# Performance work log

Measured on AMD Instinct MI355X. Metric: run time of the kernel, lower is better.

## Reference

```python
import jax, jax.numpy as jnp
import numpy as np

HIDDEN = 2048
HEADS = 16
HEAD_DIM = HIDDEN // HEADS  # 128
B, S = 2, 2048


def setup_inputs() -> dict:
    key = jax.random.key(0)
    ks = jax.random.split(key, 9)
    s_in = 1.0 / np.sqrt(HIDDEN)
    return {
        "X": jax.random.normal(ks[0], (B, S, HIDDEN), dtype=jnp.float32),
        "attention_mask": jnp.ones((B, S, S), dtype=jnp.int32),
        "Wq": jax.random.uniform(ks[1], (HIDDEN, HIDDEN), jnp.float32, -s_in, s_in),
        "bq": jax.random.uniform(ks[2], (HIDDEN,), jnp.float32, -s_in, s_in),
        "Wk": jax.random.uniform(ks[3], (HIDDEN, HEAD_DIM), jnp.float32, -s_in, s_in),
        "bk": jax.random.uniform(ks[4], (HEAD_DIM,), jnp.float32, -s_in, s_in),
        "Wv": jax.random.uniform(ks[5], (HIDDEN, HEAD_DIM), jnp.float32, -s_in, s_in),
        "bv": jax.random.uniform(ks[6], (HEAD_DIM,), jnp.float32, -s_in, s_in),
        "Wo": jax.random.uniform(ks[7], (HIDDEN, HIDDEN), jnp.float32, -s_in, s_in),
        "bo": jax.random.uniform(ks[8], (HIDDEN,), jnp.float32, -s_in, s_in),
    }


def reference(X, attention_mask, Wq, bq, Wk, bk, Wv, bv, Wo, bo):
    b, s, _ = X.shape
    # Projections
    Q = X @ Wq + bq                      # (B, S, H*D)
    K = X @ Wk + bk                      # (B, S, D)  shared across heads (MQA)
    V = X @ Wv + bv                      # (B, S, D)
    Q = Q.reshape(b, s, HEADS, HEAD_DIM).transpose(0, 2, 1, 3)  # (B, H, S, D)
    scale = 1.0 / jnp.sqrt(jnp.float32(HEAD_DIM))
    # QK^T with shared K head
    scores = jnp.einsum('bhqd,bkd->bhqk', Q, K) * scale          # (B, H, S, S)
    scores = jnp.where(attention_mask[:, None, :, :] == 0, -jnp.inf, scores)
    attn = jax.nn.softmax(scores, axis=-1)
    # dropout_rate = 0.0 (eval) -> identity
    out = jnp.einsum('bhqk,bkd->bhqd', attn, V)                  # (B, H, S, D)
    out = out.transpose(0, 2, 1, 3).reshape(b, s, HIDDEN)        # (B, S, hidden)
    return out @ Wo + bo
```

## Files before the change

kernel.cpp:

```cpp
#include <hip/hip_runtime.h>
#include <cstdint>
#include <cstddef>

#define HIDDEN 2048
#define HEADS 16
#define HD 128
#define BSZ 2
#define SEQ 2048
#define MTOT (BSZ * SEQ)
#define NQKV (HIDDEN + 2 * HD)
#define SL2E 0.12751743f

typedef unsigned short ushort_t;
typedef __attribute__((ext_vector_type(8))) __bf16 bf16x8;
typedef __attribute__((ext_vector_type(4))) float f32x4;

typedef __attribute__((address_space(3))) unsigned int as3_u32;
typedef __attribute__((address_space(1))) const unsigned int as1_u32;

__device__ __forceinline__ ushort_t f2bf(float x) {
  union { float f; unsigned u; } v; v.f = x;
  unsigned r = v.u + 0x7fffu + ((v.u >> 16) & 1u);
  return (ushort_t)(r >> 16);
}
__device__ __forceinline__ ushort_t f2bf_trunc(float x) {
  union { float f; unsigned u; } v; v.f = x;
  return (ushort_t)(v.u >> 16);
}

__device__ __forceinline__ void gld16(const void* g, void* lds) {
  __builtin_amdgcn_global_load_lds((as1_u32*)g, (as3_u32*)lds, 16, 0, 0);
}

__global__ __launch_bounds__(256) void cvt_bf16_kernel(
    const float* __restrict__ in, ushort_t* __restrict__ out, int n4) {
  int i = blockIdx.x * 256 + threadIdx.x;
  if (i >= n4) return;
  float4 v = ((const float4*)in)[i];
  ushort4 o;
  o.x = f2bf(v.x); o.y = f2bf(v.y); o.z = f2bf(v.z); o.w = f2bf(v.w);
  ((ushort4*)out)[i] = o;
}

__global__ __launch_bounds__(256) void cvtT_qkv_kernel(
    const float* __restrict__ Wq, const float* __restrict__ Wk,
    const float* __restrict__ Wv, ushort_t* __restrict__ WT) {
  __shared__ float tile[32][36];
  const int t = threadIdx.x;
  const int nb = blockIdx.x * 32, kb = blockIdx.y * 32;
  const float* W; int N, nc; float scale;
  if (nb < HIDDEN)            { W = Wq; N = HIDDEN; nc = nb;               scale = SL2E; }
  else if (nb < HIDDEN + HD)  { W = Wk; N = HD;     nc = nb - HIDDEN;      scale = 1.f; }
  else                        { W = Wv; N = HD;     nc = nb - HIDDEN - HD; scale = 1.f; }
  {
    int row = t >> 3, c4 = (t & 7) << 2;
    float4 v = *(const float4*)(W + (size_t)(kb + row) * N + nc + c4);
    tile[row][c4] = v.x * scale; tile[row][c4 + 1] = v.y * scale;
    tile[row][c4 + 2] = v.z * scale; tile[row][c4 + 3] = v.w * scale;
  }
  __syncthreads();
  {
    int nl = t >> 3, k4 = (t & 7) << 2;
    ushort4 o;
    o.x = f2bf(tile[k4 + 0][nl]); o.y = f2bf(tile[k4 + 1][nl]);
    o.z = f2bf(tile[k4 + 2][nl]); o.w = f2bf(tile[k4 + 3][nl]);
    *(ushort4*)(WT + (size_t)(nb + nl) * HIDDEN + kb + k4) = o;
  }
}

__global__ __launch_bounds__(256) void cvtT_kernel(
    const float* __restrict__ W, ushort_t* __restrict__ WT, int K, int N) {
  __shared__ float tile[32][36];
  const int t = threadIdx.x;
  const int kb = blockIdx.y * 32, nb = blockIdx.x * 32;
  {
    int row = t >> 3, c4 = (t & 7) << 2;
    float4 v = *(const float4*)(W + (size_t)(kb + row) * N + nb + c4);
    tile[row][c4] = v.x; tile[row][c4 + 1] = v.y;
    tile[row][c4 + 2] = v.z; tile[row][c4 + 3] = v.w;
  }
  __syncthreads();
  {
    int nl = t >> 3, k4 = (t & 7) << 2;
    ushort4 o;
    o.x = f2bf(tile[k4 + 0][nl]); o.y = f2bf(tile[k4 + 1][nl]);
    o.z = f2bf(tile[k4 + 2][nl]); o.w = f2bf(tile[k4 + 3][nl]);
    *(ushort4*)(WT + (size_t)(nb + nl) * K + kb + k4) = o;
  }
}

__global__ __launch_bounds__(256) void transpose_v_kernel(
    const ushort_t* __restrict__ Vin, ushort_t* __restrict__ Vt) {
  __shared__ ushort_t tile[32][40];
  const int t = threadIdx.x;
  const int rb = blockIdx.x * 32, cb = blockIdx.y * 32;
  {
    int row = t >> 3, c4 = (t & 7) << 2;
    ushort4 v = *(const ushort4*)(Vin + (size_t)(rb + row) * NQKV + cb + c4);
    tile[row][c4] = v.x; tile[row][c4 + 1] = v.y;
    tile[row][c4 + 2] = v.z; tile[row][c4 + 3] = v.w;
  }
  __syncthreads();
  {
    int dl = t >> 3, r4 = (t & 7) << 2;
    ushort4 o;
    o.x = tile[r4 + 0][dl]; o.y = tile[r4 + 1][dl];
    o.z = tile[r4 + 2][dl]; o.w = tile[r4 + 3][dl];
    *(ushort4*)(Vt + (size_t)(cb + dl) * MTOT + rb + r4) = o;
  }
}

__global__ void concat_bias_kernel(const float* __restrict__ bq,
                                   const float* __restrict__ bk,
                                   const float* __restrict__ bv,
                                   float* __restrict__ o) {
  int i = blockIdx.x * 256 + threadIdx.x;
  if (i >= NQKV) return;
  o[i] = (i < HIDDEN) ? bq[i] * SL2E
       : (i < HIDDEN + HD ? bk[i - HIDDEN] : bv[i - HIDDEN - HD]);
}

__global__ __launch_bounds__(256) void mask_flags_kernel(
    const int* __restrict__ mask, int* __restrict__ flags) {
  const int kt = blockIdx.x, qt = blockIdx.y, b = blockIdx.z;
  const int t = threadIdx.x;
  int allv = 1, anyv = 0;
  const size_t base = (size_t)b * SEQ * SEQ + (size_t)qt * 128 * SEQ + kt * 64;
  for (int i = t; i < 2048; i += 256) {
    const int row = i >> 4, c4 = (i & 15) << 2;
    const int4 v = *(const int4*)(mask + base + (size_t)row * SEQ + c4);
    const int nz = (v.x != 0) & (v.y != 0) & (v.z != 0) & (v.w != 0);
    const int nzany = (v.x != 0) | (v.y != 0) | (v.z != 0) | (v.w != 0);
    allv &= nz; anyv |= nzany;
  }
  const int wAll = __all(allv), wAny = __any(anyv);
  __shared__ int sA[4], sO[4];
  if ((t & 63) == 0) { sA[t >> 6] = wAll; sO[t >> 6] = wAny; }
  __syncthreads();
  if (t == 0) {
    const int A = sA[0] & sA[1] & sA[2] & sA[3];
    const int O = sO[0] | sO[1] | sO[2] | sO[3];
    flags[(b * 16 + qt) * 32 + kt] = A ? 2 : (O ? 1 : 0);
  }
}

template <int OUTF32>
__global__ __launch_bounds__(256) void gemm_mfma(
    const ushort_t* __restrict__ A, const ushort_t* __restrict__ Bt,
    const float* __restrict__ bias, void* __restrict__ C,
    int M, int N, int K, int nm_per_xcd) {
  __shared__ ushort_t As[2][128 * 64];
  __shared__ ushort_t Bs[2][128 * 64];
  const int t = threadIdx.x;
  const int w = t >> 6, l = t & 63;
  const int id = blockIdx.x;
  const int xcd = id & 7, j = id >> 3;
  const int mt = xcd * nm_per_xcd + (j % nm_per_xcd);
  const int nt = j / nm_per_xcd;
  const int mb = mt * 128, nb = nt * 128;
  const int wm = (w >> 1) * 64, wn = (w & 1) * 64;
  const int fl = l & 15, g = l >> 4;
  const int srow = l >> 3, cphys = l & 7;

  f32x4 acc[4][4];
#pragma unroll
  for (int i = 0; i < 4; ++i)
#pragma unroll
    for (int jj = 0; jj < 4; ++jj) acc[i][jj] = (f32x4){0.f, 0.f, 0.f, 0.f};

#pragma unroll
  for (int jj = 0; jj < 4; ++jj) {
    const int inst = w * 4 + jj;
    const int row = inst * 8 + srow;
    const int clog = cphys ^ (row & 7);
    gld16(A + (size_t)(mb + row) * K + clog * 8, &As[0][inst * 512]);
    gld16(Bt + (size_t)(nb + row) * K + clog * 8, &Bs[0][inst * 512]);
  }

  int cur = 0;
  for (int k0 = 0; k0 < K; k0 += 64) {
    __syncthreads();
    if (k0 + 64 < K) {
#pragma unroll
      for (int jj = 0; jj < 4; ++jj) {
        const int inst = w * 4 + jj;
        const int row = inst * 8 + srow;
        const int clog = cphys ^ (row & 7);
        gld16(A + (size_t)(mb + row) * K + k0 + 64 + clog * 8,
              &As[cur ^ 1][inst * 512]);
        gld16(Bt + (size_t)(nb + row) * K + k0 + 64 + clog * 8,
              &Bs[cur ^ 1][inst * 512]);
      }
    }
    const ushort_t* Ac = &As[cur][0];
    const ushort_t* Bc = &Bs[cur][0];
#pragma unroll
    for (int s = 0; s < 2; ++s) {
      bf16x8 af[4], bfr[4];
#pragma unroll
      for (int i = 0; i < 4; ++i) {
        const int m = wm + i * 16 + fl;
        af[i] = *(const bf16x8*)&Ac[m * 64 + (((s << 2) + g) ^ (m & 7)) * 8];
        const int n = wn + i * 16 + fl;
        bfr[i] = *(const bf16x8*)&Bc[n * 64 + (((s << 2) + g) ^ (n & 7)) * 8];
      }
#pragma unroll
      for (int i = 0; i < 4; ++i)
#pragma unroll
        for (int jj = 0; jj < 4; ++jj)
          acc[i][jj] = __builtin_amdgcn_mfma_f32_16x16x32_bf16(
              af[i], bfr[jj], acc[i][jj], 0, 0, 0);
    }
    cur ^= 1;
  }

#pragma unroll
  for (int jj = 0; jj < 4; ++jj) {
    const int col = nb + wn + jj * 16 + fl;
    const float bv = bias[col];
#pragma unroll
    for (int i = 0; i < 4; ++i) {
      const int row0 = mb + wm + i * 16 + g * 4;
#pragma unroll
      for (int r = 0; r < 4; ++r) {
        const float val = acc[i][jj][r] + bv;
        if (OUTF32)
          ((float*)C)[(size_t)(row0 + r) * N + col] = val;
        else
          ((ushort_t*)C)[(size_t)(row0 + r) * N + col] = f2bf(val);
      }
    }
  }
}

__global__ __launch_bounds__(256, 2) void flash_mfma(
    const ushort_t* __restrict__ QKV,
    const ushort_t* __restrict__ Vt,
    const int* __restrict__ mask,
    const int* __restrict__ flags,
    ushort_t* __restrict__ Ab)
{
  __shared__ ushort_t Kbuf[2][64 * 128];
  __shared__ ushort_t Vts[144 * 64];
  __shared__ ushort_t Ps[128 * 72];

  const int qt = blockIdx.x, h = blockIdx.y, b = blockIdx.z;
  const int t = threadIdx.x, w = t >> 6, l = t & 63;
  const int fl = l & 15, g = l >> 4;
  const int qbase = qt * 128;

  bf16x8 qf[2][4];
#pragma unroll
  for (int im = 0; im < 2; ++im) {
    const int qrow = qbase + w * 32 + im * 16 + fl;
#pragma unroll
    for (int ks = 0; ks < 4; ++ks)
      qf[im][ks] = *(const bf16x8*)(QKV + (size_t)(b * SEQ + qrow) * NQKV +
                                    h * HD + ks * 32 + g * 8);
  }

  if (t < 128) {
    const int row = 128 + (t >> 3), ch = t & 7;
    const ushort_t v = (row == 128) ? (ushort_t)0x3F80 : (ushort_t)0;
#pragma unroll
    for (int j = 0; j < 8; ++j) Vts[row * 64 + ch * 8 + j] = v;
  }

#pragma unroll
  for (int j = 0; j < 4; ++j) {
    const int inst = w * 4 + j;
    const int krow = inst * 4 + (l >> 4);
    const int ck = (l & 15) ^ (krow & 15);
    gld16(QKV + (size_t)(b * SEQ + krow) * NQKV + HIDDEN + ck * 8,
          &Kbuf[0][inst * 512]);
  }

  const size_t mbase = (size_t)b * SEQ * SEQ;
  const int qrowc0 = qbase + w * 32 + g * 4;

  f32x4 oacc[2][9];
#pragma unroll
  for (int im = 0; im < 2; ++im)
#pragma unroll
    for (int d = 0; d < 9; ++d) oacc[im][d] = (f32x4){0.f, 0.f, 0.f, 0.f};

  int cur = 0;
  for (int kt = 0; kt < SEQ / 64; ++kt) {
    const int kbase = kt * 64;
    const int flag = flags[((b * 16 + qt) << 5) + kt];
    __syncthreads();

#pragma unroll
    for (int j = 0; j < 4; ++j) {
      const int inst = w * 4 + j;
      const int drow = inst * 8 + (l >> 3);
      const int cv = (l & 7) ^ (drow & 7);
      gld16(Vt + (size_t)drow * MTOT + b * SEQ + kbase + cv * 8,
            &Vts[inst * 512]);
    }
    {
      const int knb = (kt + 1 < SEQ / 64) ? (kbase + 64) : kbase;
#pragma unroll
      for (int j = 0; j < 4; ++j) {
        const int inst = w * 4 + j;
        const int krow = inst * 4 + (l >> 4);
        const int ck = (l & 15) ^ (krow & 15);
        gld16(QKV + (size_t)(b * SEQ + knb + krow) * NQKV + HIDDEN + ck * 8,
              &Kbuf[cur ^ 1][inst * 512]);
      }
    }

    const ushort_t* Kc = &Kbuf[cur][0];
    f32x4 sc[2][4];
#pragma unroll
    for (int im = 0; im < 2; ++im)
#pragma unroll
      for (int ct = 0; ct < 4; ++ct) sc[im][ct] = (f32x4){0.f, 0.f, 0.f, 0.f};
#pragma unroll
    for (int ks = 0; ks < 4; ++ks) {
#pragma unroll
      for (int ct = 0; ct < 4; ++ct) {
        const int key = ct * 16 + fl;
        const bf16x8 kf =
            *(const bf16x8*)&Kc[key * 128 + ((ks * 4 + g) ^ (key & 15)) * 8];
        sc[0][ct] = __builtin_amdgcn_mfma_f32_16x16x32_bf16(qf[0][ks], kf,
                                                            sc[0][ct], 0, 0, 0);
        sc[1][ct] = __builtin_amdgcn_mfma_f32_16x16x32_bf16(qf[1][ks], kf,
                                                            sc[1][ct], 0, 0, 0);
      }
    }

    if (flag != 2) {
#pragma unroll
      for (int im = 0; im < 2; ++im) {
        const int qrc = qrowc0 + im * 16;
#pragma unroll
        for (int ct = 0; ct < 4; ++ct)
#pragma unroll
          for (int r = 0; r < 4; ++r) {
            const int mv =
                mask[mbase + (size_t)(qrc + r) * SEQ + kbase + ct * 16 + fl];
            if (!mv) sc[im][ct][r] = -1e30f;
          }
      }
    }

#pragma unroll
    for (int im = 0; im < 2; ++im)
#pragma unroll
      for (int ct = 0; ct < 4; ++ct)
#pragma unroll
        for (int r = 0; r < 4; ++r) {
          const float p = __builtin_amdgcn_exp2f(sc[im][ct][r]);
          Ps[(w * 32 + im * 16 + g * 4 + r) * 72 + ct * 16 + fl] =
              f2bf_trunc(p);
        }
    __syncthreads();

    bf16x8 pf[2][2];
#pragma unroll
    for (int im = 0; im < 2; ++im)
#pragma unroll
      for (int ks = 0; ks < 2; ++ks)
        pf[im][ks] = *(const bf16x8*)&Ps[(w * 32 + im * 16 + fl) * 72 +
                                         ks * 32 + g * 8];
#pragma unroll
    for (int dt = 0; dt < 9; ++dt) {
      const int drow = dt * 16 + fl;
#pragma unroll
      for (int ks = 0; ks < 2; ++ks) {
        const bf16x8 vf =
            *(const bf16x8*)&Vts[drow * 64 + ((ks * 4 + g) ^ (drow & 7)) * 8];
        oacc[0][dt] = __builtin_amdgcn_mfma_f32_16x16x32_bf16(pf[0][ks], vf,
                                                              oacc[0][dt], 0, 0, 0);
        oacc[1][dt] = __builtin_amdgcn_mfma_f32_16x16x32_bf16(pf[1][ks], vf,
                                                              oacc[1][dt], 0, 0, 0);
      }
    }
    cur ^= 1;
  }

#pragma unroll
  for (int im = 0; im < 2; ++im) {
#pragma unroll
    for (int r = 0; r < 4; ++r) {
      const float lsum = __shfl(oacc[im][8][r], (l & 48), 64);
      const float invl = 1.0f / lsum;
      const int row = b * SEQ + qrowc0 + im * 16 + r;
#pragma unroll
      for (int dt = 0; dt < 8; ++dt) {
        const int col = h * HD + dt * 16 + fl;
        Ab[(size_t)row * HIDDEN + col] = f2bf(oacc[im][dt][r] * invl);
      }
    }
  }
}

extern "C" void kernel_launch(void* const* d_in, const int* in_sizes, int n_in,
                              void* d_out, int out_size, void* d_ws, size_t ws_size,
                              hipStream_t stream) {
  const float* X  = (const float*)d_in[0];
  const int* mask = (const int*)d_in[1];
  const float* Wq = (const float*)d_in[2];
  const float* bq = (const float*)d_in[3];
  const float* Wk = (const float*)d_in[4];
  const float* bk = (const float*)d_in[5];
  const float* Wv = (const float*)d_in[6];
  const float* bv = (const float*)d_in[7];
  const float* Wo = (const float*)d_in[8];
  const float* bo = (const float*)d_in[9];
  float* out = (float*)d_out;

  char* p = (char*)d_ws;
  ushort_t* QKVb = (ushort_t*)p; p += (size_t)MTOT * NQKV * 2;
  ushort_t* Xb   = (ushort_t*)p; p += (size_t)MTOT * HIDDEN * 2;
  ushort_t* WT   = (ushort_t*)p; p += (size_t)NQKV * HIDDEN * 2;
  ushort_t* WoT  = (ushort_t*)p; p += (size_t)HIDDEN * HIDDEN * 2;
  ushort_t* Vt   = (ushort_t*)p; p += (size_t)HD * MTOT * 2;
  float* biasQKV = (float*)p;    p += 4096;
  int* flags     = (int*)p;      p += BSZ * 16 * 32 * 4;
  ushort_t* Ab = Xb;

  cvt_bf16_kernel<<<(MTOT * HIDDEN / 4 + 255) / 256, 256, 0, stream>>>(
      X, Xb, MTOT * HIDDEN / 4);
  cvtT_qkv_kernel<<<dim3(NQKV / 32, HIDDEN / 32), 256, 0, stream>>>(
      Wq, Wk, Wv, WT);
  cvtT_kernel<<<dim3(HIDDEN / 32, HIDDEN / 32), 256, 0, stream>>>(
      Wo, WoT, HIDDEN, HIDDEN);
  concat_bias_kernel<<<(NQKV + 255) / 256, 256, 0, stream>>>(bq, bk, bv, biasQKV);
  mask_flags_kernel<<<dim3(32, 16, BSZ), 256, 0, stream>>>(mask, flags);

  gemm_mfma<0><<<dim3((MTOT / 128) * (NQKV / 128)), 256, 0, stream>>>(
      Xb, WT, biasQKV, QKVb, MTOT, NQKV, HIDDEN, (MTOT / 128) / 8);
  transpose_v_kernel<<<dim3(MTOT / 32, HD / 32), 256, 0, stream>>>(
      QKVb + HIDDEN + HD, Vt);
  flash_mfma<<<dim3(SEQ / 128, HEADS, BSZ), 256, 0, stream>>>(
      QKVb, Vt, mask, flags, Ab);
  gemm_mfma<1><<<dim3((MTOT / 128) * (HIDDEN / 128)), 256, 0, stream>>>(
      Ab, WoT, bo, out, MTOT, HIDDEN, HIDDEN, (MTOT / 128) / 8);
}
```

Before: 349.3 us.

## Double-buffer V tiles, swizzle P, drop mid-loop barrier, keep ones in registers

Adds a second V buffer so the next V tile is prefetched together with the next K tile instead of being loaded at the top of each iteration. The P tile is stored with an XOR swizzle instead of padding, and the barrier between writing and reading P is removed because each wave only reads back its own rows. The row-sum ones column now comes from a register fragment rather than extra shared-memory rows. This uses more LDS for the V double buffer, and removing the barrier depends on the intra-wave ordering of the P store and load.

```diff
diff --git a/kernel.cpp b/kernel.cpp
--- a/kernel.cpp
+++ b/kernel.cpp
@@ -241,8 +241,8 @@
     ushort_t* __restrict__ Ab)
 {
   __shared__ ushort_t Kbuf[2][64 * 128];
-  __shared__ ushort_t Vts[144 * 64];
-  __shared__ ushort_t Ps[128 * 72];
+  __shared__ ushort_t Vbuf[2][128 * 64];
+  __shared__ ushort_t Ps[128 * 64];
 
   const int qt = blockIdx.x, h = blockIdx.y, b = blockIdx.z;
   const int t = threadIdx.x, w = t >> 6, l = t & 63;
@@ -259,11 +259,11 @@
                                     h * HD + ks * 32 + g * 8);
   }
 
-  if (t < 128) {
-    const int row = 128 + (t >> 3), ch = t & 7;
-    const ushort_t v = (row == 128) ? (ushort_t)0x3F80 : (ushort_t)0;
-#pragma unroll
-    for (int j = 0; j < 8; ++j) Vts[row * 64 + ch * 8 + j] = v;
+  bf16x8 onesf;
+  {
+    const ushort_t ov = (fl == 0) ? (ushort_t)0x3F80 : (ushort_t)0;
+#pragma unroll
+    for (int jj = 0; jj < 8; ++jj) ((ushort_t*)&onesf)[jj] = ov;
   }
 
 #pragma unroll
@@ -273,6 +273,9 @@
     const int ck = (l & 15) ^ (krow & 15);
     gld16(QKV + (size_t)(b * SEQ + krow) * NQKV + HIDDEN + ck * 8,
           &Kbuf[0][inst * 512]);
+    const int drow = inst * 8 + (l >> 3);
+    const int cv = (l & 7) ^ (drow & 7);
+    gld16(Vt + (size_t)drow * MTOT + b * SEQ + cv * 8, &Vbuf[0][inst * 512]);
   }
 
   const size_t mbase = (size_t)b * SEQ * SEQ;
@@ -290,14 +293,6 @@
     const int flag = flags[((b * 16 + qt) << 5) + kt];
     __syncthreads();
 
-#pragma unroll
-    for (int j = 0; j < 4; ++j) {
-      const int inst = w * 4 + j;
-      const int drow = inst * 8 + (l >> 3);
-      const int cv = (l & 7) ^ (drow & 7);
-      gld16(Vt + (size_t)drow * MTOT + b * SEQ + kbase + cv * 8,
-            &Vts[inst * 512]);
-    }
     {
       const int knb = (kt + 1 < SEQ / 64) ? (kbase + 64) : kbase;
 #pragma unroll
@@ -307,6 +302,10 @@
         const int ck = (l & 15) ^ (krow & 15);
         gld16(QKV + (size_t)(b * SEQ + knb + krow) * NQKV + HIDDEN + ck * 8,
               &Kbuf[cur ^ 1][inst * 512]);
+        const int drow = inst * 8 + (l >> 3);
+        const int cv = (l & 7) ^ (drow & 7);
+        gld16(Vt + (size_t)drow * MTOT + b * SEQ + knb + cv * 8,
+              &Vbuf[cur ^ 1][inst * 512]);
       }
     }
 
@@ -352,30 +351,41 @@
 #pragma unroll
         for (int r = 0; r < 4; ++r) {
           const float p = __builtin_amdgcn_exp2f(sc[im][ct][r]);
-          Ps[(w * 32 + im * 16 + g * 4 + r) * 72 + ct * 16 + fl] =
+          const int row = w * 32 + im * 16 + g * 4 + r;
+          Ps[row * 64 + (((ct << 1) + (fl >> 3)) ^ (row & 7)) * 8 + (fl & 7)] =
               f2bf_trunc(p);
         }
-    __syncthreads();
 
     bf16x8 pf[2][2];
 #pragma unroll
-    for (int im = 0; im < 2; ++im)
+    for (int im = 0; im < 2; ++im) {
+      const int prow = w * 32 + im * 16 + fl;
 #pragma unroll
       for (int ks = 0; ks < 2; ++ks)
-        pf[im][ks] = *(const bf16x8*)&Ps[(w * 32 + im * 16 + fl) * 72 +
-                                         ks * 32 + g * 8];
-#pragma unroll
-    for (int dt = 0; dt < 9; ++dt) {
+        pf[im][ks] = *(const bf16x8*)&Ps[prow * 64 +
+                                         (((ks << 2) + g) ^ (fl & 7)) * 8];
+    }
+
+    const ushort_t* Vc = &Vbuf[cur][0];
+#pragma unroll
+    for (int dt = 0; dt < 8; ++dt) {
       const int drow = dt * 16 + fl;
 #pragma unroll
       for (int ks = 0; ks < 2; ++ks) {
         const bf16x8 vf =
-            *(const bf16x8*)&Vts[drow * 64 + ((ks * 4 + g) ^ (drow & 7)) * 8];
+            *(const bf16x8*)&Vc[drow * 64 + ((ks * 4 + g) ^ (drow & 7)) * 8];
         oacc[0][dt] = __builtin_amdgcn_mfma_f32_16x16x32_bf16(pf[0][ks], vf,
                                                               oacc[0][dt], 0, 0, 0);
         oacc[1][dt] = __builtin_amdgcn_mfma_f32_16x16x32_bf16(pf[1][ks], vf,
                                                               oacc[1][dt], 0, 0, 0);
       }
+    }
+#pragma unroll
+    for (int ks = 0; ks < 2; ++ks) {
+      oacc[0][8] = __builtin_amdgcn_mfma_f32_16x16x32_bf16(pf[0][ks], onesf,
+                                                           oacc[0][8], 0, 0, 0);
+      oacc[1][8] = __builtin_amdgcn_mfma_f32_16x16x32_bf16(pf[1][ks], onesf,
+                                                           oacc[1][8], 0, 0, 0);
     }
     cur ^= 1;
   }
```

After: 346.0 us. No clear change (-0.9%).
